# Optimization experiments

Measured on AMD Instinct MI355X. Metric: run time of the kernel, lower is better.

Reference implementation:

```python
import jax, jax.numpy as jnp
import numpy as np

WINDOW_SHAPE = (12, 12, 32)  # (win_x, win_y, win_z)
GROUP_SIZE = 69
SHIFT = True


def setup_inputs() -> dict:
    rng = np.random.default_rng(0)
    Z, Y, X = 32, 512, 512
    batch_size = 8
    counts = [250000 + 37 * i + (i % 3) for i in range(batch_size)]  # non-multiples of GROUP_SIZE
    grid = Z * Y * X
    rows = []
    for b, n in enumerate(counts):
        lin = rng.choice(grid, size=n, replace=False)  # unique voxels per batch -> unique sort keys
        z = lin // (Y * X)
        y = (lin // X) % Y
        x = lin % X
        rows.append(np.stack([np.full(n, b), z, y, x], axis=1))
    coords = jnp.asarray(np.concatenate(rows, axis=0).astype(np.int32))
    return {"coords": coords, "batch_size": batch_size, "sparse_shape": (Z, Y, X)}


def reference(coords, batch_size, sparse_shape):
    g = GROUP_SIZE
    win_x, win_y, win_z = WINDOW_SHAPE
    sz, sy, sx = sparse_shape
    coords = coords.astype(jnp.int32)
    N = coords.shape[0]

    # ---- per-batch counts and (padded) start offsets (coords sorted by batch id) ----
    counts = jnp.bincount(coords[:, 0], length=batch_size).astype(jnp.int32)
    bs = jnp.concatenate([jnp.zeros(1, jnp.int32), jnp.cumsum(counts).astype(jnp.int32)])
    counts_p = ((counts + g - 1) // g) * g  # rounded up to multiple of group_size
    bsp = jnp.concatenate([jnp.zeros(1, jnp.int32), jnp.cumsum(counts_p).astype(jnp.int32)])
    Np = int(bsp[-1])  # padded total (eager; output length is data-dependent by construction)

    # ---- win2flat: original index -> padded position ----
    pb = coords[:, 0]  # batch of each point
    win2flat = jnp.arange(N, dtype=jnp.int32) + (bsp[:-1] - bs[:-1])[pb]

    # ---- flat2win: padded position -> original index (vectorized form of the torch loop) ----
    j = jnp.arange(Np, dtype=jnp.int32)
    b = (jnp.searchsorted(bsp, j, side='right') - 1).astype(jnp.int32)  # batch of padded pos
    off = bsp[b] - bs[b]
    num = counts[b]
    num_p = counts_p[b]
    r = num % g
    has_pad = num != num_p
    tail_start = jnp.where(has_pad, bsp[b + 1] - g + r, bsp[b + 1])
    in_tail = j >= tail_start
    multi_group = num_p != g
    val_multi = j - g - off                       # copy previous group's entries
    t = j - tail_start
    val_single = bs[b] + (t % jnp.maximum(num, 1))  # wrap-around repeat of batch elements
    flat2win = jnp.where(in_tail, jnp.where(multi_group, val_multi, val_single), j - off)

    # ---- window sort keys (win_version == 'v2') ----
    shift_x, shift_y, shift_z = (win_x // 2, win_y // 2, win_z // 2) if SHIFT else (0, 0, 0)
    mwx = int(np.ceil(sx / win_x) + 1)
    mwy = int(np.ceil(sy / win_y) + 1)
    mwz = int(np.ceil(sz / win_z) + 1)
    mps = mwx * mwy * mwz  # max windows per sample

    x = coords[:, 3] + shift_x
    y = coords[:, 2] + shift_y
    z = coords[:, 1] + shift_z
    wx, wy, wz = x // win_x, y // win_y, z // win_z
    cx, cy, cz = x % win_x, y % win_y, z % win_z

    bwi_x = coords[:, 0] * mps + wx * (mwy * mwz) + wy * mwz + wz
    bwi_y = coords[:, 0] * mps + wy * (mwx * mwz) + wx * mwz + wz

    vol = win_x * win_y * win_z
    vx = bwi_x * vol + cx * (win_y * win_z) + cy * win_z + cz
    vy = bwi_y * vol + cy * (win_x * win_z) + cx * win_z + cz

    x_map = jnp.argsort(vx).astype(jnp.int32)
    y_map = jnp.argsort(vy).astype(jnp.int32)

    return flat2win, win2flat, x_map, y_map
```

## Files before the change

### kernel.cpp

```cpp
#include <hip/hip_runtime.h>
#include <stdint.h>

#define G       69
#define BATCH   8
#define MPS     3872
#define VOL     4608
#define NBUK    1089
#define NB2     2178
#define B_WORDS 4096
#define BT      1024
#define CT      256
#define RT      512
#define NBLK    256

#define C_COUNTS 0
#define C_BS     8
#define C_CP     17
#define C_BSP    25
#define C_DONE   34

#define BSWZ(w) ((w) ^ (((w) >> 4) & 15))

__device__ __forceinline__ void keys_from_coord(int4 c, unsigned& kx, unsigned& ky) {
    int b  = c.x;
    int zz = c.y + 16;
    int yy = c.z + 6;
    int xx = c.w + 6;
    int wx = xx / 12, cx = xx - wx*12;
    int wy = yy / 12, cy = yy - wy*12;
    int wz = zz >> 5, cz = zz & 31;
    int bwx = b*MPS + wx*88 + wy*2 + wz;
    int bwy = b*MPS + wy*88 + wx*2 + wz;
    kx = (unsigned)(bwx*VOL + cx*384 + cy*32 + cz);
    ky = (unsigned)(bwy*VOL + cy*384 + cx*32 + cz);
}

__device__ __forceinline__ unsigned wave_iscan(unsigned x, int lane) {
    #pragma unroll
    for (int d = 1; d < 64; d <<= 1) {
        unsigned u = __shfl_up(x, d, 64);
        if (lane >= d) x += u;
    }
    return x;
}

__global__ __launch_bounds__(BT) void hist_kernel(const int4* __restrict__ coords, int N, int chunk,
                            int* __restrict__ ctrl, unsigned* __restrict__ histMat) {
    __shared__ unsigned h[NB2];
    __shared__ int hb[BATCH];
    int t = threadIdx.x, blk = blockIdx.x;
    for (int k = t; k < NB2; k += BT) h[k] = 0u;
    if (t < BATCH) hb[t] = 0;
    __syncthreads();
    int start = blk * chunk;
    int end   = min(start + chunk, N);
    int c0=0,c1=0,c2=0,c3=0,c4=0,c5=0,c6=0,c7=0;
    for (int i = start + t; i < end; i += BT) {
        int4 c = coords[i];
        int b = c.x;
        c0 += (b==0); c1 += (b==1); c2 += (b==2); c3 += (b==3);
        c4 += (b==4); c5 += (b==5); c6 += (b==6); c7 += (b==7);
        unsigned kx, ky;
        keys_from_coord(c, kx, ky);
        atomicAdd(&h[kx >> 17], 1u);
        atomicAdd(&h[NBUK + (ky >> 17)], 1u);
    }
    if (c0) atomicAdd(&hb[0],c0);  if (c1) atomicAdd(&hb[1],c1);
    if (c2) atomicAdd(&hb[2],c2);  if (c3) atomicAdd(&hb[3],c3);
    if (c4) atomicAdd(&hb[4],c4);  if (c5) atomicAdd(&hb[5],c5);
    if (c6) atomicAdd(&hb[6],c6);  if (c7) atomicAdd(&hb[7],c7);
    __syncthreads();
    for (int k = t; k < NB2; k += BT) histMat[(size_t)blk * NB2 + k] = h[k];
    if (t < BATCH && hb[t]) atomicAdd(&ctrl[C_COUNTS + t], hb[t]);
}

__global__ __launch_bounds__(CT) void colscan_kernel(int* __restrict__ ctrl,
                               unsigned* __restrict__ histMat,
                               unsigned* __restrict__ totals,
                               unsigned* __restrict__ recStart) {
    int t = threadIdx.x;
    int k = blockIdx.x * CT + t;
    if (k < NB2) {
        unsigned run = 0;
        for (int b = 0; b < NBLK; b += 16) {
            unsigned v[16];
            #pragma unroll
            for (int u = 0; u < 16; u++) v[u] = histMat[(size_t)(b+u)*NB2 + k];
            #pragma unroll
            for (int u = 0; u < 16; u++) { histMat[(size_t)(b+u)*NB2 + k] = run; run += v[u]; }
        }
        totals[k] = run;
    }
    __shared__ int s_last;
    __threadfence();
    __syncthreads();
    if (t == 0) {
        int d = atomicAdd(&ctrl[C_DONE], 1);
        s_last = (d == (int)gridDim.x - 1);
    }
    __syncthreads();
    if (!s_last) return;
    __threadfence();

    __shared__ unsigned warpsum[CT/64];
    __shared__ unsigned s_carry;
    int lane = t & 63, wid = t >> 6;
    if (t == 0) s_carry = 0u;
    __syncthreads();
    for (int base = 0; base < NB2; base += CT) {
        int idx = base + t;
        unsigned v = (idx < NB2) ? totals[idx] : 0u;
        unsigned x = wave_iscan(v, lane);
        if (lane == 63) warpsum[wid] = x;
        __syncthreads();
        if (wid == 0) {
            unsigned v2 = (lane < CT/64) ? warpsum[lane] : 0u;
            unsigned x2 = wave_iscan(v2, lane);
            if (lane < CT/64) warpsum[lane] = x2;
        }
        __syncthreads();
        unsigned excl = s_carry + (wid ? warpsum[wid-1] : 0u) + x - v;
        unsigned roundTot = warpsum[CT/64 - 1];
        if (idx < NB2) recStart[idx] = excl;
        __syncthreads();
        if (t == 0) s_carry += roundTot;
        __syncthreads();
    }
    if (t == 0) {
        recStart[NB2] = s_carry;
        int bs = 0, bsp = 0;
        ctrl[C_BS] = 0; ctrl[C_BSP] = 0;
        for (int b = 0; b < BATCH; b++) {
            int n  = ctrl[C_COUNTS + b];
            int np = ((n + G - 1) / G) * G;
            ctrl[C_CP + b] = np;
            bs += n; bsp += np;
            ctrl[C_BS + b + 1]  = bs;
            ctrl[C_BSP + b + 1] = bsp;
        }
    }
}

__global__ __launch_bounds__(BT) void bin_kernel(const int4* __restrict__ coords, int N, int chunk, int Np,
                           const int* __restrict__ ctrl,
                           const unsigned* __restrict__ recStart,
                           const unsigned* __restrict__ histMat,
                           uint2* __restrict__ rec,
                           int* __restrict__ w2f,
                           int* __restrict__ f2w) {
    __shared__ unsigned cur[NB2];
    __shared__ int s_off[BATCH];
    __shared__ int s_bs[BATCH+1], s_bsp[BATCH+1], s_cnt[BATCH], s_cp[BATCH];
    int t = threadIdx.x, blk = blockIdx.x;
    if (t < BATCH) {
        s_off[t] = ctrl[C_BSP+t] - ctrl[C_BS+t];
        s_cnt[t] = ctrl[C_COUNTS+t];
        s_cp[t]  = ctrl[C_CP+t];
    }
    if (t < BATCH+1) { s_bs[t] = ctrl[C_BS+t]; s_bsp[t] = ctrl[C_BSP+t]; }
    for (int k = t; k < NB2; k += BT)
        cur[k] = recStart[k] + histMat[(size_t)blk * NB2 + k];
    __syncthreads();
    int start = blk * chunk;
    int end   = min(start + chunk, N);
    for (int i = start + t; i < end; i += BT) {
        int4 c = coords[i];
        w2f[i] = i + s_off[c.x];
        unsigned kx, ky;
        keys_from_coord(c, kx, ky);
        unsigned px = atomicAdd(&cur[kx >> 17], 1u);
        rec[px] = make_uint2(kx, (unsigned)i);
        unsigned py = atomicAdd(&cur[NBUK + (ky >> 17)], 1u);
        rec[py] = make_uint2(ky, (unsigned)i);
    }
    int gs = (int)gridDim.x * BT;
    for (int j = blk*BT + t; j < Np; j += gs) {
        int b = 0;
        #pragma unroll
        for (int k = 1; k < BATCH; k++) b += (j >= s_bsp[k]);
        int off  = s_bsp[b] - s_bs[b];
        int num  = s_cnt[b], nump = s_cp[b];
        int r    = num % G;
        int tail_start = (num != nump) ? (s_bsp[b+1] - G + r) : s_bsp[b+1];
        int v;
        if (j < tail_start)       v = j - off;
        else if (nump != G)       v = j - G - off;
        else { int tt = j - tail_start; int m = num > 0 ? num : 1; v = s_bs[b] + tt % m; }
        f2w[j] = v;
    }
}

__global__ __launch_bounds__(RT) void rank_kernel(const uint2* __restrict__ rec,
                            const unsigned* __restrict__ recStart, int N,
                            int* __restrict__ xmap, int* __restrict__ ymap) {
    int b = blockIdx.x;
    unsigned start = recStart[b], end = recStart[b+1];
    int cnt = (int)(end - start);
    if (cnt == 0) return;
    int map = (b >= NBUK);
    __shared__ unsigned bits[B_WORDS];
    __shared__ unsigned short pref[B_WORDS];
    __shared__ unsigned wsum[RT/64];
    int t = threadIdx.x;
    #pragma unroll
    for (int k = 0; k < B_WORDS/RT; k++) bits[t + RT*k] = 0u;
    __syncthreads();
    for (int j = t; j < cnt; j += RT) {
        unsigned key = rec[start + j].x;
        unsigned local = key & 131071u;
        atomicOr(&bits[BSWZ(local >> 5)], 1u << (local & 31));
    }
    __syncthreads();
    int base = t * (B_WORDS/RT);
    unsigned w[B_WORDS/RT];
    unsigned s = 0;
    #pragma unroll
    for (int k = 0; k < B_WORDS/RT; k++) { w[k] = bits[BSWZ(base + k)]; s += __popc(w[k]); }
    int lane = t & 63, wid = t >> 6;
    unsigned x = wave_iscan(s, lane);
    if (lane == 63) wsum[wid] = x;
    __syncthreads();
    unsigned add = 0;
    #pragma unroll
    for (int q = 0; q < RT/64 - 1; q++) add += (wid > q) ? wsum[q] : 0u;
    unsigned excl = add + x - s;
    #pragma unroll
    for (int k = 0; k < B_WORDS/RT; k++) {
        pref[BSWZ(base + k)] = (unsigned short)excl;
        excl += __popc(w[k]);
    }
    __syncthreads();
    int* __restrict__ out = map ? ymap : xmap;
    unsigned rankBase = start - (map ? (unsigned)N : 0u);
    for (int j = t; j < cnt; j += RT) {
        uint2 r = rec[start + j];
        unsigned local = r.x & 131071u;
        unsigned wd = local >> 5, bt = local & 31u;
        unsigned sw = BSWZ(wd);
        unsigned rank = rankBase + (unsigned)pref[sw] + __popc(bits[sw] & ((1u << bt) - 1u));
        out[rank] = (int)r.y;
    }
}

extern "C" void kernel_launch(void* const* d_in, const int* in_sizes, int n_in,
                              void* d_out, int out_size, void* d_ws, size_t ws_size,
                              hipStream_t stream) {
    const int* coords = (const int*)d_in[0];
    int N  = in_sizes[0] / 4;
    int Np = out_size - 3 * N;
    int chunk = (N + NBLK - 1) / NBLK;

    char* ws = (char*)d_ws;
    int*      ctrl     = (int*)(ws + 0);
    unsigned* totals   = (unsigned*)(ws + 256);
    unsigned* recStart = (unsigned*)(ws + 8968);
    unsigned* histMat  = (unsigned*)(ws + 17696);
    uint2*    rec      = (uint2*)(ws + 2247968);

    int* out  = (int*)d_out;
    int* f2w  = out;
    int* w2f  = out + Np;
    int* xmap = out + Np + N;
    int* ymap = out + Np + 2*N;

    hipMemsetAsync(ctrl, 0, 256, stream);

    hist_kernel<<<NBLK, BT, 0, stream>>>((const int4*)coords, N, chunk, ctrl, histMat);
    colscan_kernel<<<(NB2 + CT - 1)/CT, CT, 0, stream>>>(ctrl, histMat, totals, recStart);
    bin_kernel<<<NBLK, BT, 0, stream>>>((const int4*)coords, N, chunk, Np, ctrl, recStart, histMat, rec, w2f, f2w);
    rank_kernel<<<NB2, RT, 0, stream>>>(rec, recStart, N, xmap, ymap);
}
```

Measured before the change: 153.1 us.

## Parallelize column scan of histogram matrix across 16 waves per column group

The column scan previously had one thread walk all 256 block rows of its column serially, with only 9 blocks of 256 threads. Each 1024-thread block now handles 64 columns: 16 waves each load and sum 16 rows, a shared-memory scan combines the wave partials, and each wave then writes its exclusive prefixes. This aims to cut the long serial latency chain and use more of the GPU, at the cost of extra shared-memory traffic and syncs. The final last-block scan now runs with 1024 threads.

After: 166.5 us. 1.09x slower.

```diff
diff --git a/kernel.cpp b/kernel.cpp
--- a/kernel.cpp
+++ b/kernel.cpp
@@ -9,7 +9,8 @@
 #define NB2     2178
 #define B_WORDS 4096
 #define BT      1024
-#define CT      256
+#define CT      1024
+#define CBLK    35
 #define RT      512
 #define NBLK    256
 
@@ -78,20 +79,40 @@
                                unsigned* __restrict__ histMat,
                                unsigned* __restrict__ totals,
                                unsigned* __restrict__ recStart) {
+    __shared__ unsigned part[16][64];
+    __shared__ int s_last;
     int t = threadIdx.x;
-    int k = blockIdx.x * CT + t;
-    if (k < NB2) {
+    int lane = t & 63, wid = t >> 6;
+    int col = blockIdx.x * 64 + lane;
+    unsigned v[16];
+    unsigned s = 0;
+    if (col < NB2) {
+        #pragma unroll
+        for (int u = 0; u < 16; u++) v[u] = histMat[(size_t)(wid*16 + u) * NB2 + col];
+        #pragma unroll
+        for (int u = 0; u < 16; u++) s += v[u];
+    }
+    part[wid][lane] = s;
+    __syncthreads();
+    if (wid == 0) {
         unsigned run = 0;
-        for (int b = 0; b < NBLK; b += 16) {
-            unsigned v[16];
-            #pragma unroll
-            for (int u = 0; u < 16; u++) v[u] = histMat[(size_t)(b+u)*NB2 + k];
-            #pragma unroll
-            for (int u = 0; u < 16; u++) { histMat[(size_t)(b+u)*NB2 + k] = run; run += v[u]; }
-        }
-        totals[k] = run;
-    }
-    __shared__ int s_last;
+        #pragma unroll
+        for (int w = 0; w < 16; w++) {
+            unsigned tmp = part[w][lane];
+            part[w][lane] = run;
+            run += tmp;
+        }
+        if (col < NB2) totals[col] = run;
+    }
+    __syncthreads();
+    if (col < NB2) {
+        unsigned excl = part[wid][lane];
+        #pragma unroll
+        for (int u = 0; u < 16; u++) {
+            histMat[(size_t)(wid*16 + u) * NB2 + col] = excl;
+            excl += v[u];
+        }
+    }
     __threadfence();
     __syncthreads();
     if (t == 0) {
@@ -104,13 +125,12 @@
 
     __shared__ unsigned warpsum[CT/64];
     __shared__ unsigned s_carry;
-    int lane = t & 63, wid = t >> 6;
     if (t == 0) s_carry = 0u;
     __syncthreads();
     for (int base = 0; base < NB2; base += CT) {
         int idx = base + t;
-        unsigned v = (idx < NB2) ? totals[idx] : 0u;
-        unsigned x = wave_iscan(v, lane);
+        unsigned vv = (idx < NB2) ? totals[idx] : 0u;
+        unsigned x = wave_iscan(vv, lane);
         if (lane == 63) warpsum[wid] = x;
         __syncthreads();
         if (wid == 0) {
@@ -119,7 +139,7 @@
             if (lane < CT/64) warpsum[lane] = x2;
         }
         __syncthreads();
-        unsigned excl = s_carry + (wid ? warpsum[wid-1] : 0u) + x - v;
+        unsigned excl = s_carry + (wid ? warpsum[wid-1] : 0u) + x - vv;
         unsigned roundTot = warpsum[CT/64 - 1];
         if (idx < NB2) recStart[idx] = excl;
         __syncthreads();
@@ -266,7 +286,7 @@
     hipMemsetAsync(ctrl, 0, 256, stream);
 
     hist_kernel<<<NBLK, BT, 0, stream>>>((const int4*)coords, N, chunk, ctrl, histMat);
-    colscan_kernel<<<(NB2 + CT - 1)/CT, CT, 0, stream>>>(ctrl, histMat, totals, recStart);
+    colscan_kernel<<<CBLK, CT, 0, stream>>>(ctrl, histMat, totals, recStart);
     bin_kernel<<<NBLK, BT, 0, stream>>>((const int4*)coords, N, chunk, Np, ctrl, recStart, histMat, rec, w2f, f2w);
     rank_kernel<<<NB2, RT, 0, stream>>>(rec, recStart, N, xmap, ymap);
 }
```
